# Performance work log

Hardware: AMD Instinct MI355X
Metric: run time of the kernel (lower is better)

The kernel has to match this reference:

```python
import jax, jax.numpy as jnp
import numpy as np

D_MODEL = 768; D_KV = 64; H = 12; D_FF = 3072; L = 2
TP = 4; SP = 16; MT = 16; MS = 4
MASK_RATE = 0.2; EPS = 1e-6
B = 256; T = 64; F = 64
ST = (T // TP) * (F // SP)  # 64 tokens


def ln(x, s, b):
    mu = jnp.mean(x, -1, keepdims=True)
    var = jnp.mean(jnp.square(x - mu), -1, keepdims=True)
    return (x - mu) * jax.lax.rsqrt(var + EPS) * s + b


def mha(x, Wq, bq, Wk, bk, Wv, bv, Wo, bo):
    Bz, S, D = x.shape
    q = (x @ Wq + bq).reshape(Bz, S, H, D_KV)
    k = (x @ Wk + bk).reshape(Bz, S, H, D_KV)
    v = (x @ Wv + bv).reshape(Bz, S, H, D_KV)
    scores = jnp.einsum('bqhd,bkhd->bhqk', q, k) * (D_KV ** -0.5)
    attn = jax.nn.softmax(scores, axis=-1)
    o = jnp.einsum('bhqk,bkhd->bqhd', attn, v).reshape(Bz, S, H * D_KV)
    return o @ Wo + bo


def setup_inputs():
    key = jax.random.key(0)
    ks = jax.random.split(key, 16)
    s = 0.02
    nrm = lambda k, shp: jax.random.normal(k, shp, jnp.float32) * s
    return {
        'inputs': jax.random.normal(ks[0], (B, T, F, 1), jnp.float32),
        'randomness': jax.random.uniform(ks[1], (B * ST, 3), jnp.float32),
        'perm': jax.random.permutation(ks[2], B * ST),
        'conv_w': nrm(ks[3], (TP, SP, 1, D_MODEL)), 'conv_b': jnp.zeros((D_MODEL,)),
        'temp_embd': nrm(ks[4], (MT, D_MODEL)), 'spec_embd': nrm(ks[5], (MS, D_MODEL)),
        'pos_ln_s': jnp.ones((D_MODEL,)), 'pos_ln_b': jnp.zeros((D_MODEL,)),
        'mask_tok': nrm(ks[6], (D_MODEL,)), 'agg_tok': nrm(ks[7], (D_MODEL,)),
        'Wq': nrm(ks[8], (L, D_MODEL, H * D_KV)), 'bq': jnp.zeros((L, H * D_KV)),
        'Wk': nrm(ks[9], (L, D_MODEL, H * D_KV)), 'bk': jnp.zeros((L, H * D_KV)),
        'Wv': nrm(ks[10], (L, D_MODEL, H * D_KV)), 'bv': jnp.zeros((L, H * D_KV)),
        'Wo': nrm(ks[11], (L, H * D_KV, D_MODEL)), 'bo': jnp.zeros((L, D_MODEL)),
        'ln1_s': jnp.ones((L, D_MODEL)), 'ln1_b': jnp.zeros((L, D_MODEL)),
        'W1': nrm(ks[12], (L, D_MODEL, D_FF)), 'b1': jnp.zeros((L, D_FF)),
        'W2': nrm(ks[13], (L, D_FF, D_MODEL)), 'b2': jnp.zeros((L, D_MODEL)),
        'ln2_s': jnp.ones((L, D_MODEL)), 'ln2_b': jnp.zeros((L, D_MODEL)),
    }


def reference(inputs, randomness, perm, conv_w, conv_b, temp_embd, spec_embd,
              pos_ln_s, pos_ln_b, mask_tok, agg_tok, Wq, bq, Wk, bk, Wv, bv,
              Wo, bo, ln1_s, ln1_b, W1, b1, W2, b2, ln2_s, ln2_b):
    # Conv2D patchify: [B, T, F, 1] -> [B, T/4, F/16, d_model]
    x = jax.lax.conv_general_dilated(
        inputs, conv_w, (TP, SP), 'VALID',
        dimension_numbers=('NHWC', 'HWIO', 'NHWC')) + conv_b
    Bz, Tt, Ss, D = x.shape
    e = x.reshape(Bz, Tt * Ss, D)  # token embeddings [B, 64, 768]
    # Vectorized BERT-style random masking (replaces the per-element sparse-scatter loop)
    sel = randomness[:, 0] <= MASK_RATE
    m = (sel & (randomness[:, 1] <= 0.8)).astype(e.dtype).reshape(Bz, Tt * Ss)
    rnd = (sel & (randomness[:, 1] > 0.8) & (randomness[:, 2] <= 0.5)).astype(e.dtype).reshape(Bz, Tt * Ss)
    shuffled = jax.lax.stop_gradient(e.reshape(-1, D))[perm].reshape(Bz, Tt * Ss, D)
    me = e * (1.0 - m - rnd)[..., None] + mask_tok * m[..., None] + shuffled * rnd[..., None]
    # Spectro-temporal position embeddings + LN
    pos = (temp_embd[:Tt, None, :] + spec_embd[None, :Ss, :]).reshape(Tt * Ss, D)
    h = ln(me + pos, pos_ln_s, pos_ln_b)
    # Prepend AGG token
    h = jnp.concatenate([jnp.broadcast_to(agg_tok, (Bz, 1, D)), h], axis=1)
    # Post-norm transformer encoder
    for l in range(L):
        a = mha(h, Wq[l], bq[l], Wk[l], bk[l], Wv[l], bv[l], Wo[l], bo[l])
        h = ln(h + a, ln1_s[l], ln1_b[l])
        f = jax.nn.gelu(h @ W1[l] + b1[l], approximate=False) @ W2[l] + b2[l]
        h = ln(h + f, ln2_s[l], ln2_b[l])
    return h  # last_hidden_states [B, 65, 768]; aggregated=h[:,0], predictions=h[:,1:]
```

## Files before the change

### kernel.cpp

```cpp
#include <hip/hip_runtime.h>
#include <hip/hip_bf16.h>
#include <math.h>

using bf16 = __hip_bfloat16;
typedef __bf16 bf16x8v __attribute__((ext_vector_type(8)));
typedef float f32x4 __attribute__((ext_vector_type(4)));
typedef unsigned short ushort4v __attribute__((ext_vector_type(4)));
typedef unsigned short ushort8v __attribute__((ext_vector_type(8)));

__device__ __forceinline__ float b2f(bf16 x) { return __bfloat162float(x); }
__device__ __forceinline__ bf16 f2b(float x) { return __float2bfloat16(x); }

__device__ __forceinline__ void gload_lds16(const void* g, void* l) {
  __builtin_amdgcn_global_load_lds(
      (__attribute__((address_space(1))) void*)(void*)g,
      (__attribute__((address_space(3))) void*)l, 16, 0, 0);
}

__device__ __forceinline__ float block_sum(float v, float* buf) {
  #pragma unroll
  for (int off = 32; off > 0; off >>= 1) v += __shfl_xor(v, off);
  __syncthreads();
  if ((threadIdx.x & 63) == 0) buf[threadIdx.x >> 6] = v;
  __syncthreads();
  return buf[0] + buf[1] + buf[2] + buf[3];
}

__global__ __launch_bounds__(256) void transpose_all_kernel(
    const float* __restrict__ Wq, const float* __restrict__ Wk,
    const float* __restrict__ Wv, const float* __restrict__ Wo,
    const float* __restrict__ W1, const float* __restrict__ W2,
    bf16* __restrict__ wqkvT, bf16* __restrict__ woT,
    bf16* __restrict__ w1T, bf16* __restrict__ w2T) {
  __shared__ float tile[32][33];
  const int tb = blockIdx.x;
  const float* src; bf16* dst; int K, N, t;
  if (tb < 4608) {
    const int job = tb / 576; t = tb % 576;
    const int l = job >> 2, c = job & 3;
    src = (c == 0 ? Wq : c == 1 ? Wk : c == 2 ? Wv : Wo) + (size_t)l * 768 * 768;
    dst = (c < 3) ? (wqkvT + (size_t)l * 2304 * 768 + (size_t)c * 768 * 768)
                  : (woT + (size_t)l * 768 * 768);
    K = 768; N = 768;
  } else if (tb < 9216) {
    const int r = tb - 4608; const int l = r / 2304; t = r % 2304;
    src = W1 + (size_t)l * 768 * 3072; dst = w1T + (size_t)l * 3072 * 768;
    K = 768; N = 3072;
  } else {
    const int r = tb - 9216; const int l = r / 2304; t = r % 2304;
    src = W2 + (size_t)l * 3072 * 768; dst = w2T + (size_t)l * 768 * 3072;
    K = 3072; N = 768;
  }
  const int nbx = N >> 5;
  const int bx = t % nbx, by = t / nbx;
  const int tx = threadIdx.x & 31, ty = threadIdx.x >> 5;
  #pragma unroll
  for (int i = 0; i < 4; ++i) {
    const int r = by * 32 + ty + i * 8;
    tile[ty + i * 8][tx] = src[(size_t)r * N + bx * 32 + tx];
  }
  __syncthreads();
  #pragma unroll
  for (int i = 0; i < 4; ++i) {
    const int r = bx * 32 + ty + i * 8;
    dst[(size_t)r * K + by * 32 + tx] = f2b(tile[tx][ty + i * 8]);
  }
}

__global__ __launch_bounds__(256) void biasqkv_kernel(
    const float* __restrict__ bq, const float* __restrict__ bk,
    const float* __restrict__ bv, float* __restrict__ out) {
  const int i = blockIdx.x * 256 + threadIdx.x;
  if (i >= 2 * 2304) return;
  const int l = i / 2304, n = i % 2304;
  float v = (n < 768) ? bq[l * 768 + n]
          : (n < 1536) ? bk[l * 768 + n - 768] : bv[l * 768 + n - 1536];
  out[i] = v;
}

__global__ __launch_bounds__(256) void patchify_kernel(
    const float* __restrict__ in, const float* __restrict__ w,
    const float* __restrict__ cb, bf16* __restrict__ e) {
  __shared__ float patch[8][64];
  const int tid = threadIdx.x;
  const int tok0 = blockIdx.x * 8;
  for (int idx = tid; idx < 512; idx += 256) {
    const int t = idx >> 6, p = idx & 63;
    const int tok = tok0 + t;
    const int b = tok >> 6, t2 = tok & 63, tt = t2 >> 2, ss = t2 & 3;
    const int kt = p >> 4, kf = p & 15;
    patch[t][p] = in[((size_t)b * 64 + tt * 4 + kt) * 64 + ss * 16 + kf];
  }
  __syncthreads();
  for (int i = 0; i < 3; ++i) {
    const int d = tid + i * 256;
    const float cbv = cb[d];
    float acc[8];
    #pragma unroll
    for (int t = 0; t < 8; ++t) acc[t] = cbv;
    for (int p = 0; p < 64; ++p) {
      const float wv = w[p * 768 + d];
      #pragma unroll
      for (int t = 0; t < 8; ++t) acc[t] += patch[t][p] * wv;
    }
    #pragma unroll
    for (int t = 0; t < 8; ++t) e[(size_t)(tok0 + t) * 768 + d] = f2b(acc[t]);
  }
}

__global__ __launch_bounds__(256) void embed_kernel(
    const bf16* __restrict__ e, const float* __restrict__ randomness,
    const int* __restrict__ perm, const float* __restrict__ temp_embd,
    const float* __restrict__ spec_embd, const float* __restrict__ pls,
    const float* __restrict__ plb, const float* __restrict__ mask_tok,
    const float* __restrict__ agg_tok, bf16* __restrict__ h) {
  __shared__ float rbuf[4];
  const int row = blockIdx.x;
  const int b = row / 65, s = row % 65;
  const int tid = threadIdx.x;
  const size_t ob = (size_t)row * 768;
  if (s == 0) {
    #pragma unroll
    for (int i = 0; i < 3; ++i) { const int d = tid + i * 256; h[ob + d] = f2b(agg_tok[d]); }
    return;
  }
  const int tok = s - 1;
  const int gt = b * 64 + tok;
  const float r0 = randomness[gt * 3 + 0];
  const float r1 = randomness[gt * 3 + 1];
  const float r2 = randomness[gt * 3 + 2];
  const bool selb = (r0 <= 0.2f);
  const bool mflag = selb && (r1 <= 0.8f);
  const bool rflag = selb && (r1 > 0.8f) && (r2 <= 0.5f);
  const int src = rflag ? perm[gt] : gt;
  const int tt = tok >> 2, ss2 = tok & 3;
  float v[3]; float sum = 0.f;
  #pragma unroll
  for (int i = 0; i < 3; ++i) {
    const int d = tid + i * 256;
    const float ev = mflag ? mask_tok[d] : b2f(e[(size_t)src * 768 + d]);
    v[i] = ev + temp_embd[tt * 768 + d] + spec_embd[ss2 * 768 + d];
    sum += v[i];
  }
  const float mu = block_sum(sum, rbuf) * (1.f / 768.f);
  float q = 0.f;
  #pragma unroll
  for (int i = 0; i < 3; ++i) { const float t = v[i] - mu; q += t * t; }
  const float rstd = rsqrtf(block_sum(q, rbuf) * (1.f / 768.f) + 1e-6f);
  #pragma unroll
  for (int i = 0; i < 3; ++i) {
    const int d = tid + i * 256;
    h[ob + d] = f2b((v[i] - mu) * rstd * pls[d] + plb[d]);
  }
}

template <int F32OUT>
__global__ __launch_bounds__(256) void resln_kernel(
    const bf16* __restrict__ x, const bf16* __restrict__ y,
    const float* __restrict__ sc, const float* __restrict__ bi,
    void* __restrict__ outp) {
  __shared__ float rbuf[4];
  const int tid = threadIdx.x;
  const size_t base = (size_t)blockIdx.x * 768;
  float v[3]; float s = 0.f;
  #pragma unroll
  for (int i = 0; i < 3; ++i) {
    const int d = tid + i * 256;
    v[i] = b2f(x[base + d]) + b2f(y[base + d]);
    s += v[i];
  }
  const float mu = block_sum(s, rbuf) * (1.f / 768.f);
  float q = 0.f;
  #pragma unroll
  for (int i = 0; i < 3; ++i) { const float t = v[i] - mu; q += t * t; }
  const float rstd = rsqrtf(block_sum(q, rbuf) * (1.f / 768.f) + 1e-6f);
  #pragma unroll
  for (int i = 0; i < 3; ++i) {
    const int d = tid + i * 256;
    const float o = (v[i] - mu) * rstd * sc[d] + bi[d];
    if (F32OUT) ((float*)outp)[base + d] = o;
    else        ((bf16*)outp)[base + d] = f2b(o);
  }
}

template <int ACT>
__global__ __launch_bounds__(256, 4) void gemmbk64_kernel(
    const unsigned short* __restrict__ A, const unsigned short* __restrict__ BT,
    const float* __restrict__ bias, bf16* __restrict__ C, int N, int K, int nbn) {
  __shared__ __align__(16) char smem[32768];

  const int nwg = gridDim.x;
  const int orig = blockIdx.x;
  const int q8 = nwg >> 3, r8 = nwg & 7;
  const int xcd = orig & 7, lin = orig >> 3;
  const int bid = (xcd < r8 ? xcd * (q8 + 1) : r8 * (q8 + 1) + (xcd - r8) * q8) + lin;
  const int bm = bid / nbn, bn = bid % nbn;

  const int tid = threadIdx.x;
  const int w = tid >> 6, lane = tid & 63;
  const int wm = (w >> 1) * 64, wn = (w & 1) * 64;
  const int frow = lane & 15;
  const int cg = lane >> 4;

  const size_t Kb = (size_t)K * 2;
  const int laneRow8 = lane >> 3;
  const int srcCB = (((lane & 7) ^ laneRow8) << 4);
  const char* gA = (const char*)A + ((size_t)bm * 128 + w * 32 + laneRow8) * Kb + srcCB;
  const char* gB = (const char*)BT + ((size_t)bn * 128 + w * 32 + laneRow8) * Kb + srcCB;

  f32x4 acc[4][4];
  #pragma unroll
  for (int i = 0; i < 4; ++i)
    #pragma unroll
    for (int j = 0; j < 4; ++j) acc[i][j] = f32x4{0.f, 0.f, 0.f, 0.f};

  char* sa = smem;
  char* sb = smem + 16384;

  auto stage = [&](int t) {
    const size_t kb = (size_t)t * 128;
    #pragma unroll
    for (int j = 0; j < 4; ++j) {
      gload_lds16(gA + (size_t)j * 8 * Kb + kb, sa + (w * 32 + j * 8) * 128);
      gload_lds16(gB + (size_t)j * 8 * Kb + kb, sb + (w * 32 + j * 8) * 128);
    }
  };

  auto compute = [&]() {
    #pragma unroll
    for (int kk = 0; kk < 2; ++kk) {
      bf16x8v aa[4], bb[4];
      #pragma unroll
      for (int m = 0; m < 4; ++m) {
        const int row = wm + m * 16 + frow;
        aa[m] = *(const bf16x8v*)(sa + row * 128 + (((4 * kk + cg) ^ (row & 7)) << 4));
      }
      #pragma unroll
      for (int n = 0; n < 4; ++n) {
        const int row = wn + n * 16 + frow;
        bb[n] = *(const bf16x8v*)(sb + row * 128 + (((4 * kk + cg) ^ (row & 7)) << 4));
      }
      __builtin_amdgcn_s_setprio(1);
      #pragma unroll
      for (int m = 0; m < 4; ++m)
        #pragma unroll
        for (int n = 0; n < 4; ++n)
          acc[m][n] = __builtin_amdgcn_mfma_f32_16x16x32_bf16(aa[m], bb[n], acc[m][n], 0, 0, 0);
      __builtin_amdgcn_s_setprio(0);
    }
  };

  const int T = K >> 6;
  for (int t = 0; t < T; ++t) {
    stage(t);
    __syncthreads();
    compute();
    __syncthreads();
  }

  bf16* cbuf = (bf16*)smem;
  float bias4[4];
  #pragma unroll
  for (int n = 0; n < 4; ++n) bias4[n] = bias[bn * 128 + wn + n * 16 + frow];
  const int rgrp = (lane >> 4) << 2;
  #pragma unroll
  for (int half = 0; half < 2; ++half) {
    if ((w >> 1) == half) {
      #pragma unroll
      for (int mf = 0; mf < 4; ++mf)
        #pragma unroll
        for (int n = 0; n < 4; ++n) {
          const int col = wn + n * 16 + frow;
          #pragma unroll
          for (int r = 0; r < 4; ++r) {
            float v = acc[mf][n][r] + bias4[n];
            if (ACT == 1) {
              const float u = 1.5957691216f * (v + 0.044715f * v * v * v);
              v = v / (1.f + __expf(-u));
            }
            cbuf[(mf * 16 + rgrp + r) * 136 + col] = f2b(v);
          }
        }
    }
    __syncthreads();
    #pragma unroll
    for (int jj = 0; jj < 4; ++jj) {
      const int idx = tid + jj * 256;
      const int rowl = idx >> 4, c = idx & 15;
      const ushort8v val = *(const ushort8v*)(cbuf + rowl * 136 + c * 8);
      *(ushort8v*)(C + ((size_t)(bm * 128 + half * 64 + rowl)) * N + (size_t)bn * 128 + c * 8) = val;
    }
    __syncthreads();
  }
}

__global__ __launch_bounds__(320) void attn_mfma_kernel(
    const bf16* __restrict__ qkv, bf16* __restrict__ ctx) {
  __shared__ __align__(16) bf16 sK[80][72];
  __shared__ __align__(16) bf16 sVt[64][104];
  __shared__ __align__(16) bf16 sP[5][16][104];
  const int b = blockIdx.x / 12, h = blockIdx.x % 12;
  const int tid = threadIdx.x;
  const int wave = tid >> 6, lane = tid & 63;
  const size_t base = ((size_t)b * 65) * 2304 + (size_t)h * 64;
  const bf16 bzero = f2b(0.f);

  for (int idx = tid; idx < 65 * 16; idx += 320) {
    const int row = idx >> 4, d4 = (idx & 15) * 4;
    const ushort4v kv = *(const ushort4v*)(qkv + base + (size_t)row * 2304 + 768 + d4);
    const ushort4v vv = *(const ushort4v*)(qkv + base + (size_t)row * 2304 + 1536 + d4);
    *(ushort4v*)&sK[row][d4] = kv;
    #pragma unroll
    for (int j = 0; j < 4; ++j) ((unsigned short*)&sVt[d4 + j][row])[0] = vv[j];
  }
  for (int idx = tid; idx < 15 * 16; idx += 320) {
    const int row = 65 + (idx >> 4), d4 = (idx & 15) * 4;
    *(ushort4v*)&sK[row][d4] = ushort4v{0, 0, 0, 0};
  }
  for (int idx = tid; idx < 64 * 31; idx += 320) {
    const int d = idx / 31, c = 65 + (idx % 31);
    sVt[d][c] = bzero;
  }
  __syncthreads();

  const int frow = lane & 15;
  const int koff = (lane >> 4) * 8;
  const int row0 = wave * 16;
  const int qrow = (row0 + frow > 64) ? 64 : (row0 + frow);
  const bf16* qptr = qkv + base + (size_t)qrow * 2304;
  const bf16x8v aq0 = *(const bf16x8v*)(qptr + koff);
  const bf16x8v aq1 = *(const bf16x8v*)(qptr + 32 + koff);

  const f32x4 z4 = {0.f, 0.f, 0.f, 0.f};
  f32x4 sacc[5];
  #pragma unroll
  for (int n = 0; n < 5; ++n) sacc[n] = z4;
  #pragma unroll
  for (int n = 0; n < 5; ++n) {
    const bf16x8v b0 = *(const bf16x8v*)&sK[n * 16 + frow][koff];
    const bf16x8v b1 = *(const bf16x8v*)&sK[n * 16 + frow][32 + koff];
    sacc[n] = __builtin_amdgcn_mfma_f32_16x16x32_bf16(aq0, b0, sacc[n], 0, 0, 0);
    sacc[n] = __builtin_amdgcn_mfma_f32_16x16x32_bf16(aq1, b1, sacc[n], 0, 0, 0);
  }

  #pragma unroll
  for (int r = 0; r < 4; ++r) {
    const int prow = ((lane >> 4) << 2) + r;
    float v[5];
    float mx = -1e30f;
    #pragma unroll
    for (int n = 0; n < 5; ++n) {
      const int col = n * 16 + frow;
      v[n] = (col < 65) ? sacc[n][r] * 0.125f : -1e30f;
      mx = fmaxf(mx, v[n]);
    }
    #pragma unroll
    for (int off = 1; off < 16; off <<= 1) mx = fmaxf(mx, __shfl_xor(mx, off));
    float sum = 0.f;
    #pragma unroll
    for (int n = 0; n < 5; ++n) { v[n] = __expf(v[n] - mx); sum += v[n]; }
    #pragma unroll
    for (int off = 1; off < 16; off <<= 1) sum += __shfl_xor(sum, off);
    const float inv = 1.f / sum;
    #pragma unroll
    for (int n = 0; n < 5; ++n)
      sP[wave][prow][n * 16 + frow] = f2b(v[n] * inv);
    sP[wave][prow][80 + frow] = bzero;
  }

  f32x4 oacc[4];
  #pragma unroll
  for (int n = 0; n < 4; ++n) oacc[n] = z4;
  #pragma unroll
  for (int kk = 0; kk < 3; ++kk) {
    const bf16x8v ap = *(const bf16x8v*)&sP[wave][frow][kk * 32 + koff];
    #pragma unroll
    for (int n = 0; n < 4; ++n) {
      const bf16x8v bv = *(const bf16x8v*)&sVt[n * 16 + frow][kk * 32 + koff];
      oacc[n] = __builtin_amdgcn_mfma_f32_16x16x32_bf16(ap, bv, oacc[n], 0, 0, 0);
    }
  }

  #pragma unroll
  for (int r = 0; r < 4; ++r) {
    const int row = row0 + ((lane >> 4) << 2) + r;
    if (row < 65) {
      bf16* op = ctx + ((size_t)b * 65 + row) * 768 + (size_t)h * 64 + frow;
      #pragma unroll
      for (int n = 0; n < 4; ++n) op[n * 16] = f2b(oacc[n][r]);
    }
  }
}

extern "C" void kernel_launch(void* const* d_in, const int* in_sizes, int n_in,
                              void* d_out, int out_size, void* d_ws, size_t ws_size,
                              hipStream_t stream) {
  (void)in_sizes; (void)n_in; (void)out_size; (void)ws_size;
  const float* inputs     = (const float*)d_in[0];
  const float* randomness = (const float*)d_in[1];
  const int*   perm       = (const int*)d_in[2];
  const float* conv_w     = (const float*)d_in[3];
  const float* conv_b     = (const float*)d_in[4];
  const float* temp_embd  = (const float*)d_in[5];
  const float* spec_embd  = (const float*)d_in[6];
  const float* pos_ln_s   = (const float*)d_in[7];
  const float* pos_ln_b   = (const float*)d_in[8];
  const float* mask_tok   = (const float*)d_in[9];
  const float* agg_tok    = (const float*)d_in[10];
  const float* Wq = (const float*)d_in[11]; const float* bq = (const float*)d_in[12];
  const float* Wk = (const float*)d_in[13]; const float* bk = (const float*)d_in[14];
  const float* Wv = (const float*)d_in[15]; const float* bv = (const float*)d_in[16];
  const float* Wo = (const float*)d_in[17]; const float* bo = (const float*)d_in[18];
  const float* ln1_s = (const float*)d_in[19]; const float* ln1_b = (const float*)d_in[20];
  const float* W1 = (const float*)d_in[21]; const float* b1 = (const float*)d_in[22];
  const float* W2 = (const float*)d_in[23]; const float* b2 = (const float*)d_in[24];
  const float* ln2_s = (const float*)d_in[25]; const float* ln2_b = (const float*)d_in[26];

  char* wsb = (char*)d_ws;
  size_t off = 0;
  auto carve = [&](size_t bytes) { char* p = wsb + off; off = (off + bytes + 255) & ~(size_t)255; return p; };
  bf16* wqkvT = (bf16*)carve((size_t)2 * 2304 * 768 * 2);
  bf16* woT   = (bf16*)carve((size_t)2 * 768 * 768 * 2);
  bf16* w1T   = (bf16*)carve((size_t)2 * 3072 * 768 * 2);
  bf16* w2T   = (bf16*)carve((size_t)2 * 768 * 3072 * 2);
  float* bqkv = (float*)carve((size_t)2 * 2304 * 4);
  bf16* ebuf  = (bf16*)carve((size_t)16640 * 768 * 2);
  bf16* hbuf  = (bf16*)carve((size_t)16640 * 768 * 2);
  bf16* qkvb  = (bf16*)carve((size_t)16640 * 2304 * 2);
  bf16* ctxb  = (bf16*)carve((size_t)16640 * 768 * 2);
  bf16* tmpb  = ebuf;
  bf16* midb  = qkvb;

  const dim3 blk(256);
  transpose_all_kernel<<<13824, blk, 0, stream>>>(Wq, Wk, Wv, Wo, W1, W2,
                                                  wqkvT, woT, w1T, w2T);
  biasqkv_kernel<<<18, blk, 0, stream>>>(bq, bk, bv, bqkv);
  patchify_kernel<<<2048, blk, 0, stream>>>(inputs, conv_w, conv_b, ebuf);
  embed_kernel<<<16640, blk, 0, stream>>>(ebuf, randomness, perm, temp_embd, spec_embd,
                                          pos_ln_s, pos_ln_b, mask_tok, agg_tok, hbuf);
  for (int l = 0; l < 2; ++l) {
    gemmbk64_kernel<0><<<130 * 18, blk, 0, stream>>>(
        (const unsigned short*)hbuf, (const unsigned short*)(wqkvT + (size_t)l * 2304 * 768),
        bqkv + l * 2304, qkvb, 2304, 768, 18);
    attn_mfma_kernel<<<256 * 12, dim3(320), 0, stream>>>(qkvb, ctxb);
    gemmbk64_kernel<0><<<130 * 6, blk, 0, stream>>>(
        (const unsigned short*)ctxb, (const unsigned short*)(woT + (size_t)l * 768 * 768),
        bo + l * 768, tmpb, 768, 768, 6);
    resln_kernel<0><<<16640, blk, 0, stream>>>(hbuf, tmpb, ln1_s + l * 768, ln1_b + l * 768, hbuf);
    gemmbk64_kernel<1><<<130 * 24, blk, 0, stream>>>(
        (const unsigned short*)hbuf, (const unsigned short*)(w1T + (size_t)l * 3072 * 768),
        b1 + l * 3072, midb, 3072, 768, 24);
    gemmbk64_kernel<0><<<130 * 6, blk, 0, stream>>>(
        (const unsigned short*)midb, (const unsigned short*)(w2T + (size_t)l * 768 * 3072),
        b2 + l * 768, tmpb, 768, 3072, 6);
    if (l == 1)
      resln_kernel<1><<<16640, blk, 0, stream>>>(hbuf, tmpb, ln2_s + l * 768, ln2_b + l * 768, d_out);
    else
      resln_kernel<0><<<16640, blk, 0, stream>>>(hbuf, tmpb, ln2_s + l * 768, ln2_b + l * 768, hbuf);
  }
}
```

Before: 846.7 us.

## Load GEMM A fragments directly from global into registers, skipping LDS

The GEMM kernel no longer stages the A tile through shared memory. Each wave now loads its A MFMA fragments straight from global memory into registers, and only B goes through LDS. This shrinks LDS use and cuts LDS reads and writes for A. In exchange, A rows are re-read by the two waves that share a row block, global loads become less coalesced (16-byte pieces across 16 rows), and load latency is exposed right before the barrier.

```diff
diff --git a/kernel.cpp b/kernel.cpp
--- a/kernel.cpp
+++ b/kernel.cpp
@@ -184,10 +184,10 @@
 }
 
 template <int ACT>
-__global__ __launch_bounds__(256, 4) void gemmbk64_kernel(
+__global__ __launch_bounds__(256, 4) void gemmaf_kernel(
     const unsigned short* __restrict__ A, const unsigned short* __restrict__ BT,
     const float* __restrict__ bias, bf16* __restrict__ C, int N, int K, int nbn) {
-  __shared__ __align__(16) char smem[32768];
+  __shared__ __align__(16) char smem[18432];
 
   const int nwg = gridDim.x;
   const int orig = blockIdx.x;
@@ -205,8 +205,8 @@
   const size_t Kb = (size_t)K * 2;
   const int laneRow8 = lane >> 3;
   const int srcCB = (((lane & 7) ^ laneRow8) << 4);
-  const char* gA = (const char*)A + ((size_t)bm * 128 + w * 32 + laneRow8) * Kb + srcCB;
   const char* gB = (const char*)BT + ((size_t)bn * 128 + w * 32 + laneRow8) * Kb + srcCB;
+  const char* gA0 = (const char*)A + ((size_t)bm * 128 + wm + frow) * Kb + cg * 16;
 
   f32x4 acc[4][4];
   #pragma unroll
@@ -214,27 +214,29 @@
     #pragma unroll
     for (int j = 0; j < 4; ++j) acc[i][j] = f32x4{0.f, 0.f, 0.f, 0.f};
 
-  char* sa = smem;
-  char* sb = smem + 16384;
-
-  auto stage = [&](int t) {
+  char* sb = smem;
+
+  auto stageB = [&](int t) {
     const size_t kb = (size_t)t * 128;
     #pragma unroll
-    for (int j = 0; j < 4; ++j) {
-      gload_lds16(gA + (size_t)j * 8 * Kb + kb, sa + (w * 32 + j * 8) * 128);
+    for (int j = 0; j < 4; ++j)
       gload_lds16(gB + (size_t)j * 8 * Kb + kb, sb + (w * 32 + j * 8) * 128);
-    }
   };
 
-  auto compute = [&]() {
+  const int T = K >> 6;
+  for (int t = 0; t < T; ++t) {
+    stageB(t);
+    bf16x8v a2[2][4];
+    const char* gAt = gA0 + (size_t)t * 128;
+    #pragma unroll
+    for (int kk = 0; kk < 2; ++kk)
+      #pragma unroll
+      for (int m = 0; m < 4; ++m)
+        a2[kk][m] = *(const bf16x8v*)(gAt + (size_t)(m * 16) * Kb + kk * 64);
+    __syncthreads();
     #pragma unroll
     for (int kk = 0; kk < 2; ++kk) {
-      bf16x8v aa[4], bb[4];
-      #pragma unroll
-      for (int m = 0; m < 4; ++m) {
-        const int row = wm + m * 16 + frow;
-        aa[m] = *(const bf16x8v*)(sa + row * 128 + (((4 * kk + cg) ^ (row & 7)) << 4));
-      }
+      bf16x8v bb[4];
       #pragma unroll
       for (int n = 0; n < 4; ++n) {
         const int row = wn + n * 16 + frow;
@@ -245,16 +247,9 @@
       for (int m = 0; m < 4; ++m)
         #pragma unroll
         for (int n = 0; n < 4; ++n)
-          acc[m][n] = __builtin_amdgcn_mfma_f32_16x16x32_bf16(aa[m], bb[n], acc[m][n], 0, 0, 0);
+          acc[m][n] = __builtin_amdgcn_mfma_f32_16x16x32_bf16(a2[kk][m], bb[n], acc[m][n], 0, 0, 0);
       __builtin_amdgcn_s_setprio(0);
     }
-  };
-
-  const int T = K >> 6;
-  for (int t = 0; t < T; ++t) {
-    stage(t);
-    __syncthreads();
-    compute();
     __syncthreads();
   }
 
@@ -439,18 +434,18 @@
   embed_kernel<<<16640, blk, 0, stream>>>(ebuf, randomness, perm, temp_embd, spec_embd,
                                           pos_ln_s, pos_ln_b, mask_tok, agg_tok, hbuf);
   for (int l = 0; l < 2; ++l) {
-    gemmbk64_kernel<0><<<130 * 18, blk, 0, stream>>>(
+    gemmaf_kernel<0><<<130 * 18, blk, 0, stream>>>(
         (const unsigned short*)hbuf, (const unsigned short*)(wqkvT + (size_t)l * 2304 * 768),
         bqkv + l * 2304, qkvb, 2304, 768, 18);
     attn_mfma_kernel<<<256 * 12, dim3(320), 0, stream>>>(qkvb, ctxb);
-    gemmbk64_kernel<0><<<130 * 6, blk, 0, stream>>>(
+    gemmaf_kernel<0><<<130 * 6, blk, 0, stream>>>(
         (const unsigned short*)ctxb, (const unsigned short*)(woT + (size_t)l * 768 * 768),
         bo + l * 768, tmpb, 768, 768, 6);
     resln_kernel<0><<<16640, blk, 0, stream>>>(hbuf, tmpb, ln1_s + l * 768, ln1_b + l * 768, hbuf);
-    gemmbk64_kernel<1><<<130 * 24, blk, 0, stream>>>(
+    gemmaf_kernel<1><<<130 * 24, blk, 0, stream>>>(
         (const unsigned short*)hbuf, (const unsigned short*)(w1T + (size_t)l * 3072 * 768),
         b1 + l * 3072, midb, 3072, 768, 24);
-    gemmbk64_kernel<0><<<130 * 6, blk, 0, stream>>>(
+    gemmaf_kernel<0><<<130 * 6, blk, 0, stream>>>(
         (const unsigned short*)midb, (const unsigned short*)(w2T + (size_t)l * 768 * 3072),
         b2 + l * 768, tmpb, 768, 3072, 6);
     if (l == 1)
```

Result: slower. 1.490 ms (+76.0%).
